# Kernel optimization log

Measured on AMD Instinct MI355X. Metric: run time of the kernel, lower is better.

Reference implementation:

```python
import jax, jax.numpy as jnp
import numpy as np

N_NODES = 50000
N_EDGES = 800000
IN_CH = 128
HID = 128
NUM_GRAPHS = 512
BN_EPS = 1e-5


def setup_inputs() -> dict:
    key = jax.random.key(0)
    ks = jax.random.split(key, 16)
    x = jax.random.normal(ks[0], (N_NODES, IN_CH), dtype=jnp.float32)
    edge_index = jax.random.randint(ks[1], (2, N_EDGES), 0, N_NODES, dtype=jnp.int64)
    batch = jnp.sort(jax.random.randint(ks[2], (N_NODES,), 0, NUM_GRAPHS, dtype=jnp.int64))

    def glorot(k, shape):
        fan_in = shape[1]
        return jax.random.normal(k, shape, dtype=jnp.float32) / jnp.sqrt(jnp.float32(fan_in))

    # SAGEConv1: lin_l (aggr path, with bias), lin_r (root path, no bias)
    W1l = glorot(ks[3], (HID, IN_CH)); b1 = jnp.zeros((HID,), jnp.float32)
    W1r = glorot(ks[4], (HID, IN_CH))
    # SAGEConv2
    W2l = glorot(ks[5], (HID, HID)); b2 = jnp.zeros((HID,), jnp.float32)
    W2r = glorot(ks[6], (HID, HID))
    # MLP tail
    lin1_w = glorot(ks[7], (HID, HID)); lin1_b = jnp.zeros((HID,), jnp.float32)
    lin2_w = glorot(ks[8], (2, HID)); lin2_b = jnp.zeros((2,), jnp.float32)
    # BatchNorm1d (eval mode, running stats)
    gamma = jnp.ones((HID,), jnp.float32)
    beta = jnp.zeros((HID,), jnp.float32)
    running_mean = jax.random.normal(ks[9], (HID,), dtype=jnp.float32) * 0.1
    running_var = jax.random.uniform(ks[10], (HID,), dtype=jnp.float32, minval=0.5, maxval=1.5)
    return {
        "x": x, "edge_index": edge_index, "batch": batch,
        "W1l": W1l, "b1": b1, "W1r": W1r,
        "W2l": W2l, "b2": b2, "W2r": W2r,
        "lin1_w": lin1_w, "lin1_b": lin1_b,
        "lin2_w": lin2_w, "lin2_b": lin2_b,
        "gamma": gamma, "beta": beta,
        "running_mean": running_mean, "running_var": running_var,
    }


def _sage_conv(x, src, dst, Wl, bl, Wr):
    # mean-aggregate neighbor features (message flows src -> dst)
    n = x.shape[0]
    agg = jax.ops.segment_sum(x[src], dst, num_segments=n)  # [N, d]
    cnt = jax.ops.segment_sum(jnp.ones((src.shape[0], 1), x.dtype), dst, num_segments=n)
    mean = agg / jnp.maximum(cnt, 1.0)
    return mean @ Wl.T + bl + x @ Wr.T


def reference(x, edge_index, batch, W1l, b1, W1r, W2l, b2, W2r,
              lin1_w, lin1_b, lin2_w, lin2_b, gamma, beta,
              running_mean, running_var):
    src, dst = edge_index[0], edge_index[1]
    h = _sage_conv(x, src, dst, W1l, b1, W1r)      # [N, HID]
    h = _sage_conv(h, src, dst, W2l, b2, W2r)      # [N, HID]
    h = jax.ops.segment_sum(h, batch, num_segments=NUM_GRAPHS)  # global_add_pool -> [G, HID]
    h = h @ lin1_w.T + lin1_b
    # BatchNorm1d in eval mode (running stats)
    h = (h - running_mean) * jax.lax.rsqrt(running_var + BN_EPS) * gamma + beta
    h = jax.nn.relu(h)
    h = h @ lin2_w.T + lin2_b                      # [G, 2]
    # Dropout is identity in eval mode
    return h
```

## Files before the change

kernel.cpp:

```cpp
#include <hip/hip_runtime.h>
#include <hip/hip_bf16.h>

#define NN 50000
#define NE 800000
#define HID 128
#define NG 512
#define BN_EPS 1e-5f

typedef __attribute__((ext_vector_type(8))) short bf16x8;
typedef __attribute__((ext_vector_type(4))) float f32x4;

__device__ __forceinline__ ushort f2bf(float f) {
    uint u = __float_as_uint(f);
    uint r = (u + 0x7fffu + ((u >> 16) & 1u)) >> 16;
    return (ushort)r;
}
__device__ __forceinline__ float bf_lo(uint v) { return __uint_as_float(v << 16); }
__device__ __forceinline__ float bf_hi(uint v) { return __uint_as_float(v & 0xffff0000u); }

#define NCH 64
#define CHE 12500
#define NRNG 4
#define HRNG 12500
#define HWORDS 6250
#define HIST_BLOCKS (NCH * NRNG)
#define CONV_BLOCKS 6250
#define WPREP_BLOCKS 32
#define POOLZ_BLOCKS 64
#define PH_GRID (HIST_BLOCKS + CONV_BLOCKS + WPREP_BLOCKS + POOLZ_BLOCKS)

__global__ __launch_bounds__(256) void prep_hist_kernel(const int* __restrict__ ei,
                                                        ushort* __restrict__ rank,
                                                        ushort* __restrict__ blockcnt,
                                                        const float* __restrict__ x,
                                                        ushort* __restrict__ xb,
                                                        const float* __restrict__ W0,
                                                        const float* __restrict__ W1,
                                                        const float* __restrict__ W2,
                                                        const float* __restrict__ W3,
                                                        ushort* __restrict__ Wp,
                                                        float* __restrict__ pooled) {
    __shared__ uint hh[HWORDS];
    uint b = blockIdx.x;
    if (b < HIST_BLOCKS) {
        int c = b >> 2;
        int r = b & 3;
        for (int i = threadIdx.x; i < HWORDS; i += 256) hh[i] = 0;
        __syncthreads();
        int base = c * CHE;
        int lo = r * HRNG;
        const int4* ev = (const int4*)(ei + NE + base);
        const int nvec = CHE / 4;
        int k4 = threadIdx.x;
        int4 cur;
        bool have = k4 < nvec;
        if (have) cur = ev[k4];
        while (have) {
            int kn = k4 + 256;
            bool hn = kn < nvec;
            int4 nxt;
            if (hn) nxt = ev[kn];
            int e0 = base + k4 * 4;
#pragma unroll
            for (int j = 0; j < 4; ++j) {
                int d = (j == 0) ? cur.x : (j == 1) ? cur.y : (j == 2) ? cur.z : cur.w;
                int local = d - lo;
                if ((unsigned)local < (unsigned)HRNG) {
                    uint sh = (local & 1) << 4;
                    uint old = atomicAdd(&hh[local >> 1], 1u << sh);
                    rank[e0 + j] = (ushort)((old >> sh) & 0xffffu);
                }
            }
            k4 = kn;
            cur = nxt;
            have = hn;
        }
        __syncthreads();
        uint* dstw = (uint*)(blockcnt + (size_t)c * NN) + r * HWORDS;
        for (int i = threadIdx.x; i < HWORDS; i += 256) dstw[i] = hh[i];
    } else if (b < HIST_BLOCKS + CONV_BLOCKS) {
        int i = (b - HIST_BLOCKS) * 256 + threadIdx.x;
        float4 v = ((const float4*)x)[i];
        ushort4 o;
        o.x = f2bf(v.x);
        o.y = f2bf(v.y);
        o.z = f2bf(v.z);
        o.w = f2bf(v.w);
        ((ushort4*)xb)[i] = o;
    } else if (b < HIST_BLOCKS + CONV_BLOCKS + WPREP_BLOCKS) {
        int wu = (b - HIST_BLOCKS - CONV_BLOCKS) * 4 + (threadIdx.x >> 6);
        if (wu >= 128) return;
        int lane = threadIdx.x & 63;
        int m = wu >> 5;
        int g = wu & 31;
        int tile = g >> 2;
        int chunk = g & 3;
        const float* W = (m == 0) ? W0 : (m == 1) ? W1 : (m == 2) ? W2 : W3;
        int col = tile * 16 + (lane & 15);
        int k0 = chunk * 32 + (lane >> 4) * 8;
        ushort* dst = Wp + ((size_t)wu * 64 + lane) * 8;
#pragma unroll
        for (int j = 0; j < 8; ++j) dst[j] = f2bf(W[col * HID + k0 + j]);
    } else {
        int i = (b - HIST_BLOCKS - CONV_BLOCKS - WPREP_BLOCKS) * 256 + threadIdx.x;
        ((float4*)pooled)[i] = make_float4(0.f, 0.f, 0.f, 0.f);
    }
}

__global__ __launch_bounds__(256) void chunkscan_kernel(ushort* __restrict__ blockcnt,
                                                        int* __restrict__ deg) {
    int t = blockIdx.x * 256 + threadIdx.x;
    if (t >= NN / 2) return;
    uint run_lo = 0, run_hi = 0;
    uint* col = (uint*)blockcnt + t;
#pragma unroll 4
    for (int c = 0; c < NCH; ++c) {
        uint w = col[(size_t)c * (NN / 2)];
        col[(size_t)c * (NN / 2)] = run_lo | (run_hi << 16);
        run_lo += w & 0xffffu;
        run_hi += w >> 16;
    }
    ((int2*)deg)[t] = make_int2((int)run_lo, (int)run_hi);
}

__global__ __launch_bounds__(256) void scan1_kernel(const int* __restrict__ deg,
                                                    int* __restrict__ row_start,
                                                    int* __restrict__ bsums, int n) {
    __shared__ int wsum[4];
    int i = blockIdx.x * 256 + threadIdx.x;
    int lane = threadIdx.x & 63;
    int wid = threadIdx.x >> 6;
    int v = (i < n) ? deg[i] : 0;
    int sc = v;
#pragma unroll
    for (int off = 1; off < 64; off <<= 1) {
        int t = __shfl_up(sc, off);
        if (lane >= off) sc += t;
    }
    if (lane == 63) wsum[wid] = sc;
    __syncthreads();
    int wpre = 0;
#pragma unroll
    for (int k = 0; k < 4; ++k) wpre += (k < wid) ? wsum[k] : 0;
    if (i < n) row_start[i] = wpre + sc - v;
    if (threadIdx.x == 255) bsums[blockIdx.x] = wpre + sc;
}

__global__ __launch_bounds__(256) void scan23_kernel(int* __restrict__ row_start,
                                                     const int* __restrict__ bsums, int n) {
    __shared__ int sred[4];
    int v = (threadIdx.x < blockIdx.x) ? bsums[threadIdx.x] : 0;
#pragma unroll
    for (int off = 32; off > 0; off >>= 1) v += __shfl_xor(v, off);
    if ((threadIdx.x & 63) == 0) sred[threadIdx.x >> 6] = v;
    __syncthreads();
    int total = sred[0] + sred[1] + sred[2] + sred[3];
    int i = blockIdx.x * 256 + threadIdx.x;
    if (i < n) row_start[i] += total;
}

__global__ __launch_bounds__(256) void fill_kernel(const int* __restrict__ ei,
                                                   const int* __restrict__ row_start,
                                                   const ushort* __restrict__ rank,
                                                   const ushort* __restrict__ blockcnt,
                                                   ushort* __restrict__ srclist) {
    int e4 = blockIdx.x * 256 + threadIdx.x;
    if (e4 >= NE / 4) return;
    int4 src = ((const int4*)ei)[e4];
    int4 dst = ((const int4*)(ei + NE))[e4];
    ushort4 rk = ((const ushort4*)rank)[e4];
    int c = e4 / (CHE / 4);
    const ushort* off = blockcnt + (size_t)c * NN;
    int p0 = row_start[dst.x] + off[dst.x] + rk.x;
    int p1 = row_start[dst.y] + off[dst.y] + rk.y;
    int p2 = row_start[dst.z] + off[dst.z] + rk.z;
    int p3 = row_start[dst.w] + off[dst.w] + rk.w;
    srclist[p0] = (ushort)src.x;
    srclist[p1] = (ushort)src.y;
    srclist[p2] = (ushort)src.z;
    srclist[p3] = (ushort)src.w;
}

__global__ __launch_bounds__(256) void aggregate_kernel(const ushort* __restrict__ feat,
                                                        const int* __restrict__ row_start,
                                                        const int* __restrict__ deg,
                                                        const ushort* __restrict__ srclist,
                                                        ushort* __restrict__ mean, int n) {
    int node = blockIdx.x * 4 + (threadIdx.x >> 6);
    if (node >= n) return;
    int lane = threadIdx.x & 63;
    int cl = lane & 15;
    int sub = lane >> 4;
    const uint4* fb = (const uint4*)feat;
    int s0 = row_start[node];
    int d = deg[node];

    float a[8];
#pragma unroll
    for (int i = 0; i < 8; ++i) a[i] = 0.f;

    int j = 0;
    for (; j + 16 <= d; j += 16) {
        int i0 = srclist[s0 + j + sub];
        int i1 = srclist[s0 + j + 4 + sub];
        int i2 = srclist[s0 + j + 8 + sub];
        int i3 = srclist[s0 + j + 12 + sub];
        uint4 v0 = fb[(size_t)i0 * 16 + cl];
        uint4 v1 = fb[(size_t)i1 * 16 + cl];
        uint4 v2 = fb[(size_t)i2 * 16 + cl];
        uint4 v3 = fb[(size_t)i3 * 16 + cl];
        a[0] += (bf_lo(v0.x) + bf_lo(v1.x)) + (bf_lo(v2.x) + bf_lo(v3.x));
        a[1] += (bf_hi(v0.x) + bf_hi(v1.x)) + (bf_hi(v2.x) + bf_hi(v3.x));
        a[2] += (bf_lo(v0.y) + bf_lo(v1.y)) + (bf_lo(v2.y) + bf_lo(v3.y));
        a[3] += (bf_hi(v0.y) + bf_hi(v1.y)) + (bf_hi(v2.y) + bf_hi(v3.y));
        a[4] += (bf_lo(v0.z) + bf_lo(v1.z)) + (bf_lo(v2.z) + bf_lo(v3.z));
        a[5] += (bf_hi(v0.z) + bf_hi(v1.z)) + (bf_hi(v2.z) + bf_hi(v3.z));
        a[6] += (bf_lo(v0.w) + bf_lo(v1.w)) + (bf_lo(v2.w) + bf_lo(v3.w));
        a[7] += (bf_hi(v0.w) + bf_hi(v1.w)) + (bf_hi(v2.w) + bf_hi(v3.w));
    }
    if (j < d) {
        int dm1 = d - 1;
        int k0 = j + sub;
        int k1 = j + 4 + sub;
        int k2 = j + 8 + sub;
        int k3 = j + 12 + sub;
        int i0 = srclist[s0 + min(k0, dm1)];
        int i1 = srclist[s0 + min(k1, dm1)];
        int i2 = srclist[s0 + min(k2, dm1)];
        int i3 = srclist[s0 + min(k3, dm1)];
        uint4 v0 = fb[(size_t)i0 * 16 + cl];
        uint4 v1 = fb[(size_t)i1 * 16 + cl];
        uint4 v2 = fb[(size_t)i2 * 16 + cl];
        uint4 v3 = fb[(size_t)i3 * 16 + cl];
        float m0 = (k0 < d) ? 1.f : 0.f;
        float m1 = (k1 < d) ? 1.f : 0.f;
        float m2 = (k2 < d) ? 1.f : 0.f;
        float m3 = (k3 < d) ? 1.f : 0.f;
        a[0] += m0 * bf_lo(v0.x) + m1 * bf_lo(v1.x) + m2 * bf_lo(v2.x) + m3 * bf_lo(v3.x);
        a[1] += m0 * bf_hi(v0.x) + m1 * bf_hi(v1.x) + m2 * bf_hi(v2.x) + m3 * bf_hi(v3.x);
        a[2] += m0 * bf_lo(v0.y) + m1 * bf_lo(v1.y) + m2 * bf_lo(v2.y) + m3 * bf_lo(v3.y);
        a[3] += m0 * bf_hi(v0.y) + m1 * bf_hi(v1.y) + m2 * bf_hi(v2.y) + m3 * bf_hi(v3.y);
        a[4] += m0 * bf_lo(v0.z) + m1 * bf_lo(v1.z) + m2 * bf_lo(v2.z) + m3 * bf_lo(v3.z);
        a[5] += m0 * bf_hi(v0.z) + m1 * bf_hi(v1.z) + m2 * bf_hi(v2.z) + m3 * bf_hi(v3.z);
        a[6] += m0 * bf_lo(v0.w) + m1 * bf_lo(v1.w) + m2 * bf_lo(v2.w) + m3 * bf_lo(v3.w);
        a[7] += m0 * bf_hi(v0.w) + m1 * bf_hi(v1.w) + m2 * bf_hi(v2.w) + m3 * bf_hi(v3.w);
    }

#pragma unroll
    for (int i = 0; i < 8; ++i) {
        float v = a[i];
        v += __shfl_xor(v, 16);
        v += __shfl_xor(v, 32);
        a[i] = v;
    }

    if (sub == 0) {
        float inv = 1.0f / fmaxf((float)d, 1.0f);
        uint4 o;
        o.x = (uint)f2bf(a[0] * inv) | ((uint)f2bf(a[1] * inv) << 16);
        o.y = (uint)f2bf(a[2] * inv) | ((uint)f2bf(a[3] * inv) << 16);
        o.z = (uint)f2bf(a[4] * inv) | ((uint)f2bf(a[5] * inv) << 16);
        o.w = (uint)f2bf(a[6] * inv) | ((uint)f2bf(a[7] * inv) << 16);
        ((uint4*)mean)[(size_t)node * 16 + cl] = o;
    }
}

template <bool POOL>
__global__ __launch_bounds__(256) void sage_gemm_mfma(const ushort* __restrict__ Amean,
                                                      const ushort* __restrict__ Aroot,
                                                      const ushort* __restrict__ WpL,
                                                      const float* __restrict__ bias,
                                                      const int* __restrict__ batch,
                                                      void* __restrict__ outv, int nwaves) {
    int w = blockIdx.x * 4 + (threadIdx.x >> 6);
    if (w >= nwaves) return;
    int lane = threadIdx.x & 63;
    int mrow = lane & 15;
    int quad = lane >> 4;
    int r0 = w * 16;

    f32x4 acc[8];
#pragma unroll
    for (int t = 0; t < 8; ++t) acc[t] = (f32x4){0.f, 0.f, 0.f, 0.f};

    const ushort* arow_m = Amean + ((size_t)(r0 + mrow)) * HID + quad * 8;
    const ushort* arow_r = Aroot + ((size_t)(r0 + mrow)) * HID + quad * 8;

#pragma unroll
    for (int half = 0; half < 2; ++half) {
        const ushort* arow = half ? arow_r : arow_m;
        const ushort* wb = WpL + (size_t)half * 16384 + (size_t)lane * 8;
#pragma unroll
        for (int c = 0; c < 4; ++c) {
            bf16x8 a = *(const bf16x8*)(arow + c * 32);
#pragma unroll
            for (int t = 0; t < 8; ++t) {
                bf16x8 b = *(const bf16x8*)(wb + (size_t)(t * 4 + c) * 512);
                acc[t] = __builtin_amdgcn_mfma_f32_16x16x32_bf16(a, b, acc[t], 0, 0, 0);
            }
        }
    }

    if (POOL) {
        float* pooled = (float*)outv;
        int rbase = r0 + quad * 4;
        int g0 = batch[rbase + 0];
        int g1 = batch[rbase + 1];
        int g2 = batch[rbase + 2];
        int g3 = batch[rbase + 3];
#pragma unroll
        for (int t = 0; t < 8; ++t) {
            int col = t * 16 + mrow;
            float bv = bias[col];
            float v0 = acc[t][0] + bv;
            float v1 = acc[t][1] + bv;
            float v2 = acc[t][2] + bv;
            float v3 = acc[t][3] + bv;
            int cg = g0;
            float s = v0;
            if (g1 == cg) s += v1; else { atomicAdd(&pooled[(size_t)cg * HID + col], s); cg = g1; s = v1; }
            if (g2 == cg) s += v2; else { atomicAdd(&pooled[(size_t)cg * HID + col], s); cg = g2; s = v2; }
            if (g3 == cg) s += v3; else { atomicAdd(&pooled[(size_t)cg * HID + col], s); cg = g3; s = v3; }
            atomicAdd(&pooled[(size_t)cg * HID + col], s);
        }
    } else {
        ushort* out = (ushort*)outv;
#pragma unroll
        for (int t = 0; t < 8; ++t) {
            int col = t * 16 + mrow;
            float bv = bias[col];
#pragma unroll
            for (int r = 0; r < 4; ++r) {
                int row = r0 + quad * 4 + r;
                out[(size_t)row * HID + col] = f2bf(acc[t][r] + bv);
            }
        }
    }
}

__global__ __launch_bounds__(128) void tail_kernel(const float* __restrict__ pooled,
                                                   const float* __restrict__ lin1_w,
                                                   const float* __restrict__ lin1_b,
                                                   const float* __restrict__ lin2_w,
                                                   const float* __restrict__ lin2_b,
                                                   const float* __restrict__ gamma,
                                                   const float* __restrict__ beta,
                                                   const float* __restrict__ rmean,
                                                   const float* __restrict__ rvar,
                                                   float* __restrict__ out) {
    __shared__ float Wt[64 * 128];
    __shared__ float p[128];
    __shared__ float tbuf[128];
    int g = blockIdx.x;
    int c = threadIdx.x;
    p[c] = pooled[g * HID + c];
    float acc = lin1_b[c];
    int kk = c & 63;
    int chalf = c >> 6;
    for (int k0 = 0; k0 < 128; k0 += 64) {
        __syncthreads();
        for (int i = 0; i < 64; ++i) {
            int crow = i * 2 + chalf;
            float v = lin1_w[crow * HID + k0 + kk];
            Wt[kk * 128 + (crow ^ (kk & 31))] = v;
        }
        __syncthreads();
#pragma unroll
        for (int k = 0; k < 64; ++k) {
            acc += p[k0 + k] * Wt[k * 128 + (c ^ (k & 31))];
        }
    }
    float v = (acc - rmean[c]) * rsqrtf(rvar[c] + BN_EPS) * gamma[c] + beta[c];
    v = fmaxf(v, 0.f);
    tbuf[c] = v;
    __syncthreads();
    int j = c >> 6;
    int lane = c & 63;
    float partial = tbuf[lane] * lin2_w[j * HID + lane] +
                    tbuf[lane + 64] * lin2_w[j * HID + lane + 64];
    for (int off = 32; off > 0; off >>= 1) partial += __shfl_down(partial, off);
    if (lane == 0) out[g * 2 + j] = partial + lin2_b[j];
}

extern "C" void kernel_launch(void* const* d_in, const int* in_sizes, int n_in,
                              void* d_out, int out_size, void* d_ws, size_t ws_size,
                              hipStream_t stream) {
    const float* x = (const float*)d_in[0];
    const int* ei = (const int*)d_in[1];
    const int* batch = (const int*)d_in[2];
    const float* W1l = (const float*)d_in[3];
    const float* b1 = (const float*)d_in[4];
    const float* W1r = (const float*)d_in[5];
    const float* W2l = (const float*)d_in[6];
    const float* b2 = (const float*)d_in[7];
    const float* W2r = (const float*)d_in[8];
    const float* lin1_w = (const float*)d_in[9];
    const float* lin1_b = (const float*)d_in[10];
    const float* lin2_w = (const float*)d_in[11];
    const float* lin2_b = (const float*)d_in[12];
    const float* gamma = (const float*)d_in[13];
    const float* beta = (const float*)d_in[14];
    const float* rmean = (const float*)d_in[15];
    const float* rvar = (const float*)d_in[16];
    float* out = (float*)d_out;

    const int N = NN, E = NE;
    const int NWAVES = N / 16;

    char* p = (char*)d_ws;
    auto carve = [&](size_t bytes) {
        void* r = (void*)p;
        p += (bytes + 255) & ~(size_t)255;
        return r;
    };
    int* deg = (int*)carve((size_t)N * 4);
    int* row_start = (int*)carve((size_t)N * 4);
    int* bsums = (int*)carve(1024 * 4);
    ushort* rank = (ushort*)carve((size_t)E * 2);
    ushort* blockcnt = (ushort*)carve((size_t)NCH * NN * 2);
    ushort* srclist = (ushort*)carve((size_t)E * 2 + 64);
    ushort* xb = (ushort*)carve((size_t)N * HID * 2);
    ushort* meanb = (ushort*)carve((size_t)N * HID * 2);
    ushort* h1 = (ushort*)carve((size_t)N * HID * 2);
    float* pooled = (float*)carve((size_t)NG * HID * 4);
    ushort* Wp = (ushort*)carve(4 * 32 * 64 * 8 * 2);

    prep_hist_kernel<<<PH_GRID, 256, 0, stream>>>(ei, rank, blockcnt, x, xb,
                                                  W1l, W1r, W2l, W2r, Wp, pooled);

    chunkscan_kernel<<<(N / 2 + 255) / 256, 256, 0, stream>>>(blockcnt, deg);

    const int scanBlocks = (N + 255) / 256;
    scan1_kernel<<<scanBlocks, 256, 0, stream>>>(deg, row_start, bsums, N);
    scan23_kernel<<<scanBlocks, 256, 0, stream>>>(row_start, bsums, N);
    fill_kernel<<<(E / 4 + 255) / 256, 256, 0, stream>>>(ei, row_start, rank, blockcnt, srclist);

    aggregate_kernel<<<(N + 3) / 4, 256, 0, stream>>>(xb, row_start, deg, srclist, meanb, N);
    sage_gemm_mfma<false><<<(NWAVES + 3) / 4, 256, 0, stream>>>(meanb, xb, Wp, b1, nullptr, h1,
                                                                NWAVES);
    aggregate_kernel<<<(N + 3) / 4, 256, 0, stream>>>(h1, row_start, deg, srclist, meanb, N);
    sage_gemm_mfma<true><<<(NWAVES + 3) / 4, 256, 0, stream>>>(meanb, h1, Wp + 32768, b2, batch,
                                                               pooled, NWAVES);
    tail_kernel<<<NG, 128, 0, stream>>>(pooled, lin1_w, lin1_b, lin2_w, lin2_b,
                                        gamma, beta, rmean, rvar, out);
}
```

Baseline: 247.6 us.

## Fuse chunk scan into scan1 and rewrite aggregation with wave-shuffled indices

The per-node chunk-prefix scan is merged into the first block-scan kernel: half the threads compute column prefixes, stash degrees in shared memory and the scan reads them from there, which removes one launch and a global round trip. The aggregation kernel now has each wave load up to 64 neighbor indices with one coalesced read and broadcast them by shuffle. Each lane then gathers one 32-bit word per neighbor, so the cross-subgroup reduction disappears. The cost is narrower per-lane loads (4 bytes instead of 16) and more shuffles, and the fused scan leaves half of each block idle during the column walk.

Result: slower. 253.6 us (+2.4%).

```diff
diff --git a/kernel.cpp b/kernel.cpp
--- a/kernel.cpp
+++ b/kernel.cpp
@@ -107,30 +107,32 @@
     }
 }
 
-__global__ __launch_bounds__(256) void chunkscan_kernel(ushort* __restrict__ blockcnt,
-                                                        int* __restrict__ deg) {
-    int t = blockIdx.x * 256 + threadIdx.x;
-    if (t >= NN / 2) return;
-    uint run_lo = 0, run_hi = 0;
-    uint* col = (uint*)blockcnt + t;
-#pragma unroll 4
-    for (int c = 0; c < NCH; ++c) {
-        uint w = col[(size_t)c * (NN / 2)];
-        col[(size_t)c * (NN / 2)] = run_lo | (run_hi << 16);
-        run_lo += w & 0xffffu;
-        run_hi += w >> 16;
-    }
-    ((int2*)deg)[t] = make_int2((int)run_lo, (int)run_hi);
-}
-
-__global__ __launch_bounds__(256) void scan1_kernel(const int* __restrict__ deg,
+__global__ __launch_bounds__(256) void scan1_kernel(ushort* __restrict__ blockcnt,
+                                                    int* __restrict__ deg,
                                                     int* __restrict__ row_start,
                                                     int* __restrict__ bsums, int n) {
     __shared__ int wsum[4];
+    __shared__ int degsh[256];
     int i = blockIdx.x * 256 + threadIdx.x;
+    int w = blockIdx.x * 128 + (int)threadIdx.x;
+    if (threadIdx.x < 128 && w < NN / 2) {
+        uint run_lo = 0, run_hi = 0;
+        uint* col = (uint*)blockcnt + w;
+#pragma unroll 4
+        for (int c = 0; c < NCH; ++c) {
+            uint x = col[(size_t)c * (NN / 2)];
+            col[(size_t)c * (NN / 2)] = run_lo | (run_hi << 16);
+            run_lo += x & 0xffffu;
+            run_hi += x >> 16;
+        }
+        degsh[2 * (int)threadIdx.x] = (int)run_lo;
+        degsh[2 * (int)threadIdx.x + 1] = (int)run_hi;
+        ((int2*)deg)[w] = make_int2((int)run_lo, (int)run_hi);
+    }
+    __syncthreads();
     int lane = threadIdx.x & 63;
     int wid = threadIdx.x >> 6;
-    int v = (i < n) ? deg[i] : 0;
+    int v = (i < n) ? degsh[threadIdx.x] : 0;
     int sc = v;
 #pragma unroll
     for (int off = 1; off < 64; off <<= 1) {
@@ -189,80 +191,38 @@
     int node = blockIdx.x * 4 + (threadIdx.x >> 6);
     if (node >= n) return;
     int lane = threadIdx.x & 63;
-    int cl = lane & 15;
-    int sub = lane >> 4;
-    const uint4* fb = (const uint4*)feat;
+    const uint* fb = (const uint*)feat;
     int s0 = row_start[node];
     int d = deg[node];
 
-    float a[8];
-#pragma unroll
-    for (int i = 0; i < 8; ++i) a[i] = 0.f;
-
-    int j = 0;
-    for (; j + 16 <= d; j += 16) {
-        int i0 = srclist[s0 + j + sub];
-        int i1 = srclist[s0 + j + 4 + sub];
-        int i2 = srclist[s0 + j + 8 + sub];
-        int i3 = srclist[s0 + j + 12 + sub];
-        uint4 v0 = fb[(size_t)i0 * 16 + cl];
-        uint4 v1 = fb[(size_t)i1 * 16 + cl];
-        uint4 v2 = fb[(size_t)i2 * 16 + cl];
-        uint4 v3 = fb[(size_t)i3 * 16 + cl];
-        a[0] += (bf_lo(v0.x) + bf_lo(v1.x)) + (bf_lo(v2.x) + bf_lo(v3.x));
-        a[1] += (bf_hi(v0.x) + bf_hi(v1.x)) + (bf_hi(v2.x) + bf_hi(v3.x));
-        a[2] += (bf_lo(v0.y) + bf_lo(v1.y)) + (bf_lo(v2.y) + bf_lo(v3.y));
-        a[3] += (bf_hi(v0.y) + bf_hi(v1.y)) + (bf_hi(v2.y) + bf_hi(v3.y));
-        a[4] += (bf_lo(v0.z) + bf_lo(v1.z)) + (bf_lo(v2.z) + bf_lo(v3.z));
-        a[5] += (bf_hi(v0.z) + bf_hi(v1.z)) + (bf_hi(v2.z) + bf_hi(v3.z));
-        a[6] += (bf_lo(v0.w) + bf_lo(v1.w)) + (bf_lo(v2.w) + bf_lo(v3.w));
-        a[7] += (bf_hi(v0.w) + bf_hi(v1.w)) + (bf_hi(v2.w) + bf_hi(v3.w));
-    }
-    if (j < d) {
-        int dm1 = d - 1;
-        int k0 = j + sub;
-        int k1 = j + 4 + sub;
-        int k2 = j + 8 + sub;
-        int k3 = j + 12 + sub;
-        int i0 = srclist[s0 + min(k0, dm1)];
-        int i1 = srclist[s0 + min(k1, dm1)];
-        int i2 = srclist[s0 + min(k2, dm1)];
-        int i3 = srclist[s0 + min(k3, dm1)];
-        uint4 v0 = fb[(size_t)i0 * 16 + cl];
-        uint4 v1 = fb[(size_t)i1 * 16 + cl];
-        uint4 v2 = fb[(size_t)i2 * 16 + cl];
-        uint4 v3 = fb[(size_t)i3 * 16 + cl];
-        float m0 = (k0 < d) ? 1.f : 0.f;
-        float m1 = (k1 < d) ? 1.f : 0.f;
-        float m2 = (k2 < d) ? 1.f : 0.f;
-        float m3 = (k3 < d) ? 1.f : 0.f;
-        a[0] += m0 * bf_lo(v0.x) + m1 * bf_lo(v1.x) + m2 * bf_lo(v2.x) + m3 * bf_lo(v3.x);
-        a[1] += m0 * bf_hi(v0.x) + m1 * bf_hi(v1.x) + m2 * bf_hi(v2.x) + m3 * bf_hi(v3.x);
-        a[2] += m0 * bf_lo(v0.y) + m1 * bf_lo(v1.y) + m2 * bf_lo(v2.y) + m3 * bf_lo(v3.y);
-        a[3] += m0 * bf_hi(v0.y) + m1 * bf_hi(v1.y) + m2 * bf_hi(v2.y) + m3 * bf_hi(v3.y);
-        a[4] += m0 * bf_lo(v0.z) + m1 * bf_lo(v1.z) + m2 * bf_lo(v2.z) + m3 * bf_lo(v3.z);
-        a[5] += m0 * bf_hi(v0.z) + m1 * bf_hi(v1.z) + m2 * bf_hi(v2.z) + m3 * bf_hi(v3.z);
-        a[6] += m0 * bf_lo(v0.w) + m1 * bf_lo(v1.w) + m2 * bf_lo(v2.w) + m3 * bf_lo(v3.w);
-        a[7] += m0 * bf_hi(v0.w) + m1 * bf_hi(v1.w) + m2 * bf_hi(v2.w) + m3 * bf_hi(v3.w);
-    }
-
-#pragma unroll
-    for (int i = 0; i < 8; ++i) {
-        float v = a[i];
-        v += __shfl_xor(v, 16);
-        v += __shfl_xor(v, 32);
-        a[i] = v;
-    }
-
-    if (sub == 0) {
-        float inv = 1.0f / fmaxf((float)d, 1.0f);
-        uint4 o;
-        o.x = (uint)f2bf(a[0] * inv) | ((uint)f2bf(a[1] * inv) << 16);
-        o.y = (uint)f2bf(a[2] * inv) | ((uint)f2bf(a[3] * inv) << 16);
-        o.z = (uint)f2bf(a[4] * inv) | ((uint)f2bf(a[5] * inv) << 16);
-        o.w = (uint)f2bf(a[6] * inv) | ((uint)f2bf(a[7] * inv) << 16);
-        ((uint4*)mean)[(size_t)node * 16 + cl] = o;
-    }
+    float a0 = 0.f, a1 = 0.f;
+    for (int jb = 0; jb < d; jb += 64) {
+        int nj = min(64, d - jb);
+        int sl = (jb + lane < d) ? (int)srclist[s0 + jb + lane] : 0;
+        int j = 0;
+        for (; j + 4 <= nj; j += 4) {
+            int i0 = __shfl(sl, j);
+            int i1 = __shfl(sl, j + 1);
+            int i2 = __shfl(sl, j + 2);
+            int i3 = __shfl(sl, j + 3);
+            uint v0 = fb[(uint)(i0 << 6) + lane];
+            uint v1 = fb[(uint)(i1 << 6) + lane];
+            uint v2 = fb[(uint)(i2 << 6) + lane];
+            uint v3 = fb[(uint)(i3 << 6) + lane];
+            a0 += (bf_lo(v0) + bf_lo(v1)) + (bf_lo(v2) + bf_lo(v3));
+            a1 += (bf_hi(v0) + bf_hi(v1)) + (bf_hi(v2) + bf_hi(v3));
+        }
+        for (; j < nj; ++j) {
+            int i0 = __shfl(sl, j);
+            uint v0 = fb[(uint)(i0 << 6) + lane];
+            a0 += bf_lo(v0);
+            a1 += bf_hi(v0);
+        }
+    }
+
+    float inv = 1.0f / fmaxf((float)d, 1.0f);
+    uint o = (uint)f2bf(a0 * inv) | ((uint)f2bf(a1 * inv) << 16);
+    ((uint*)mean)[(uint)(node << 6) + lane] = o;
 }
 
 template <bool POOL>
@@ -428,10 +388,8 @@
     prep_hist_kernel<<<PH_GRID, 256, 0, stream>>>(ei, rank, blockcnt, x, xb,
                                                   W1l, W1r, W2l, W2r, Wp, pooled);
 
-    chunkscan_kernel<<<(N / 2 + 255) / 256, 256, 0, stream>>>(blockcnt, deg);
-
     const int scanBlocks = (N + 255) / 256;
-    scan1_kernel<<<scanBlocks, 256, 0, stream>>>(deg, row_start, bsums, N);
+    scan1_kernel<<<scanBlocks, 256, 0, stream>>>(blockcnt, deg, row_start, bsums, N);
     scan23_kernel<<<scanBlocks, 256, 0, stream>>>(row_start, bsums, N);
     fill_kernel<<<(E / 4 + 255) / 256, 256, 0, stream>>>(ei, row_start, rank, blockcnt, srclist);
 
```
